# Performance work log

Hardware: AMD Instinct MI355X
Metric: run time of the kernel (lower is better)

## Reference

```python
import jax, jax.numpy as jnp
import numpy as np

N_HEADS = 16
D_MODEL = 512
HEAD_DIM = D_MODEL // N_HEADS
SCALE = 1.0 / (HEAD_DIM ** 0.5)
R = 4  # LSREF radius -> window = step = 2*r = 8


def _layernorm(x, g, b, eps=1e-5):
    m = x.mean(axis=-1, keepdims=True)
    v = x.var(axis=-1, keepdims=True)
    return (x - m) / jnp.sqrt(v + eps) * g + b


def _mha(q_in, k_in, v_in, wq, bq, wk, bk, wv, bv, wo, bo):
    # Informer FullAttention(mask_flag=False), AttentionLayer(mix=False), eval mode (no dropout)
    B, L, _ = q_in.shape
    S = k_in.shape[1]
    q = (q_in @ wq.T + bq).reshape(B, L, N_HEADS, HEAD_DIM)
    k = (k_in @ wk.T + bk).reshape(B, S, N_HEADS, HEAD_DIM)
    v = (v_in @ wv.T + bv).reshape(B, S, N_HEADS, HEAD_DIM)
    scores = jnp.einsum('blhe,bshe->bhls', q, k) * SCALE
    A = jax.nn.softmax(scores, axis=-1)
    out = jnp.einsum('bhls,bshd->blhd', A, v).reshape(B, L, D_MODEL)
    return out @ wo.T + bo


def setup_inputs() -> dict:
    key = jax.random.key(0)
    ks = jax.random.split(key, 32)
    B, L, C, GL, DFF = 4, 1024, 512, 4096, 2048

    def w(k, shape, s=0.02):
        return (jax.random.normal(k, shape, jnp.float32) * s).astype(jnp.float32)

    inp = {
        'x': jax.random.normal(ks[0], (B, L, C), jnp.float32),
        'global_feat': jax.random.normal(ks[1], (B, C, GL), jnp.float32),
        'conv_w': w(ks[2], (C, C)), 'conv_b': jnp.zeros((C,), jnp.float32),
        'sa_wq': w(ks[3], (C, C)), 'sa_bq': jnp.zeros((C,), jnp.float32),
        'sa_wk': w(ks[4], (C, C)), 'sa_bk': jnp.zeros((C,), jnp.float32),
        'sa_wv': w(ks[5], (C, C)), 'sa_bv': jnp.zeros((C,), jnp.float32),
        'sa_wo': w(ks[6], (C, C)), 'sa_bo': jnp.zeros((C,), jnp.float32),
        'ca_wq': w(ks[7], (C, C)), 'ca_bq': jnp.zeros((C,), jnp.float32),
        'ca_wk': w(ks[8], (C, C)), 'ca_bk': jnp.zeros((C,), jnp.float32),
        'ca_wv': w(ks[9], (C, C)), 'ca_bv': jnp.zeros((C,), jnp.float32),
        'ca_wo': w(ks[10], (C, C)), 'ca_bo': jnp.zeros((C,), jnp.float32),
        'ffn_w1': w(ks[11], (DFF, C)), 'ffn_b1': jnp.zeros((DFF,), jnp.float32),
        'ffn_w2': w(ks[12], (C, DFF)), 'ffn_b2': jnp.zeros((C,), jnp.float32),
        'n1_g': jnp.ones((C,), jnp.float32), 'n1_b': jnp.zeros((C,), jnp.float32),
        'n2_g': jnp.ones((C,), jnp.float32), 'n2_b': jnp.zeros((C,), jnp.float32),
        'n3_g': jnp.ones((C,), jnp.float32), 'n3_b': jnp.zeros((C,), jnp.float32),
    }
    return inp


def reference(x, global_feat, conv_w, conv_b,
              sa_wq, sa_bq, sa_wk, sa_bk, sa_wv, sa_bv, sa_wo, sa_bo,
              ca_wq, ca_bq, ca_wk, ca_bk, ca_wv, ca_bv, ca_wo, ca_bo,
              ffn_w1, ffn_b1, ffn_w2, ffn_b2,
              n1_g, n1_b, n2_g, n2_b, n3_g, n3_b):
    # --- sliding_window_gaussian: non-overlapping windows (step == window == 2r) ---
    B, C, GL = global_feat.shape
    win_sz = 2 * R
    nw = (GL - win_sz) // win_sz + 1
    win = global_feat[:, :, :nw * win_sz].reshape(B, C, nw, win_sz)
    # torch.norm over a keepdim=1 axis is just |max - min|
    res = jnp.abs(win.max(axis=-1) - win.min(axis=-1)) + 1e-6  # [B, C, nw]
    # conv1d kernel size 1 == channelwise linear, then relu
    res = jax.nn.relu(jnp.einsum('oc,bcn->bon', conv_w, res) + conv_b[None, :, None])
    cross = res  # [B, 512, nw=512] consumed as [B, S, d_model]

    # --- CrossPyramidFusion: one Informer-style layer (self-attn, cross-attn, conv FFN) ---
    h = x + _mha(x, x, x, sa_wq, sa_bq, sa_wk, sa_bk, sa_wv, sa_bv, sa_wo, sa_bo)
    h = _layernorm(h, n1_g, n1_b)
    h = h + _mha(h, cross, cross, ca_wq, ca_bq, ca_wk, ca_bk, ca_wv, ca_bv, ca_wo, ca_bo)
    h = _layernorm(h, n2_g, n2_b)
    y = jax.nn.gelu(h @ ffn_w1.T + ffn_b1, approximate=False)
    y = y @ ffn_w2.T + ffn_b2
    out = _layernorm(h + y, n3_g, n3_b)
    return out.transpose(0, 2, 1)  # [B, 512, L]
```

## Files before the change

### kernel.cpp

```cpp
#include <hip/hip_runtime.h>
#include <hip/hip_bf16.h>
#include <math.h>

#define SCALE_Q 0.25504522f

typedef unsigned short u16;
typedef unsigned int u32;
typedef __attribute__((ext_vector_type(8))) short bshort8;
typedef __attribute__((ext_vector_type(4))) short sshort4;
typedef __attribute__((ext_vector_type(4))) float f32x4;
typedef __attribute__((ext_vector_type(4))) u32 u32x4;

__device__ inline u16 f2b(float f) {
    union { float f; uint32_t u; } c;
    c.f = f;
    uint32_t u = c.u;
    return (u16)((u + 0x7fffu + ((u >> 16) & 1u)) >> 16);
}

__device__ __forceinline__ float b2f(u16 b) {
    union { u32 u; float f; } c;
    c.u = (u32)b << 16;
    return c.f;
}

__device__ __forceinline__ u32 cvtpk(float a, float b) {
    u32 r;
    asm("v_cvt_pk_bf16_f32 %0, %1, %2" : "=v"(r) : "v"(a), "v"(b));
    return r;
}

__device__ __forceinline__ float exp2c(float s) {
    float c = fminf(s, 100.f);
    float r;
    asm("v_exp_f32 %0, %1" : "=v"(r) : "v"(c));
    return r;
}

__device__ inline void gload_lds16(const void* g, void* lds) {
    __builtin_amdgcn_global_load_lds(
        (const __attribute__((address_space(1))) void*)g,
        (__attribute__((address_space(3))) void*)lds, 16, 0, 0);
}

struct WSrc { const float* p[12]; };
__global__ __launch_bounds__(256) void prep_kernel(WSrc s, u16* __restrict__ dst,
                                                   const float* __restrict__ G,
                                                   u16* __restrict__ Rt) {
    int bid = blockIdx.x;
    if (bid < 256) {
        __shared__ u16 T[64][72];
        int b = bid >> 6, c0 = ((bid >> 3) & 7) << 6, n0 = (bid & 7) << 6;
        int t = threadIdx.x;
        int n = t & 63, cq = t >> 6;
        const float* Gb = G + (long)b * 512 * 4096;
        #pragma unroll
        for (int i = 0; i < 16; i++) {
            int c = i * 4 + cq;
            const float4* p = (const float4*)(Gb + (long)(c0 + c) * 4096 + (n0 + n) * 8);
            float4 a = p[0], bb = p[1];
            float mx = fmaxf(fmaxf(fmaxf(a.x, a.y), fmaxf(a.z, a.w)),
                             fmaxf(fmaxf(bb.x, bb.y), fmaxf(bb.z, bb.w)));
            float mn = fminf(fminf(fminf(a.x, a.y), fminf(a.z, a.w)),
                             fminf(fminf(bb.x, bb.y), fminf(bb.z, bb.w)));
            T[n][c] = f2b(fabsf(mx - mn) + 1e-6f);
        }
        __syncthreads();
        int nr = t >> 2, ck = (t & 3) << 4;
        u16* o = Rt + ((long)(b * 512 + n0 + nr) << 9) + c0 + ck;
        *(bshort8*)o = *(const bshort8*)&T[nr][ck];
        *(bshort8*)(o + 8) = *(const bshort8*)&T[nr][ck + 8];
    } else {
        long e = ((long)(bid - 256) * 256 + threadIdx.x) * 4;
        if (e >= 6553600) return;
        int w; long base;
        if (e < 2359296)      { w = (int)(e >> 18); base = (long)w << 18; }
        else if (e < 3407872) { w = 9;  base = 2359296; }
        else if (e < 4456448) { w = 10; base = 3407872; }
        else                  { w = 11; base = 4456448; }
        float4 v = *(const float4*)(s.p[w] + (e - base));
        dst[e + 0] = f2b(v.x); dst[e + 1] = f2b(v.y);
        dst[e + 2] = f2b(v.z); dst[e + 3] = f2b(v.w);
    }
}

struct GArg {
    const u16* A; const u16* Bt;
    const float* bias; const u16* Rres;
    void* Cout;
    int N, K;
    long sA, sB, sC;
    u16* D1; u16* D2;
    const float* bias1; const float* bias2;
    int gx, gy;
};

template <int BIASMODE, int ACT, bool RESID, int OUTMODE>
__device__ __forceinline__ void gemm_epilogue_elem(
    float v, int row, int col, int N, long zoff,
    const float* bias, const u16* Rres, void* Cout,
    u16* D1, u16* D2, const float* bias1, const float* bias2) {
    if (OUTMODE == 3) {
        int grp = col >> 9, c = col & 511;
        float bb = (grp == 0) ? bias[c] : (grp == 1) ? bias1[c] : bias2[c];
        float vv = v + bb;
        if (grp == 0)
            ((u16*)Cout)[(long)row * 512 + c] = f2b(vv * SCALE_Q);
        else if (grp == 1)
            D1[(long)row * 512 + c] = f2b(vv);
        else
            D2[((long)((row >> 10) * 512 + c) << 10) + (row & 1023)] = f2b(vv);
    } else if (OUTMODE == 4) {
        int grp = col >> 9, c = col & 511;
        float vv = v + ((grp == 0) ? bias[c] : bias1[c]);
        if (grp == 0)
            ((u16*)Cout)[(long)row * 512 + c] = f2b(vv);
        else
            D2[((long)((row >> 9) * 512 + c) << 9) + (row & 511)] = f2b(vv);
    } else {
        if (BIASMODE == 1) v += bias[col];
        if (BIASMODE == 2) v += bias[row];
        if (ACT == 1) v = fmaxf(v, 0.f);
        if (ACT == 2) v = 0.5f * v * (1.f + erff(v * 0.70710678118654752f));
        if (ACT == 3) v *= SCALE_Q;
        if (RESID) v += b2f(Rres[(long)row * N + col]);
        long off = zoff + (long)row * N + col;
        if (OUTMODE == 1) ((u16*)Cout)[off] = f2b(v);
        else              ((float*)Cout)[off] = v;
    }
}

template <int BIASMODE, int ACT, bool RESID, int OUTMODE>
__device__ __forceinline__ void bgemm64_body(
    u16* AsB, u16* BsB, const GArg& ga, int bx, int by, int bz) {
    const u16* A  = ga.A + (long)bz * ga.sA;
    const u16* Bt = ga.Bt + (long)bz * ga.sB;
    int K = ga.K, N = ga.N;
    int tid = threadIdx.x;
    int lane = tid & 63, wv = tid >> 6;
    int wr = wv >> 1, wc = wv & 1;
    int m0 = bx * 64, n0 = by * 64;
    f32x4 acc[2][2] = {};
    int srow = lane >> 3;
    int selem = ((lane & 7) ^ srow) << 3;

    auto STAGE = [&](int buf, int k0) {
        #pragma unroll
        for (int i = 0; i < 2; i++) {
            int roff = i * 32 + wv * 8;
            gload_lds16(A + (long)(m0 + roff + srow) * K + k0 + selem,
                        (char*)(AsB + buf * 4096) + roff * 128);
            gload_lds16(Bt + (long)(n0 + roff + srow) * K + k0 + selem,
                        (char*)(BsB + buf * 4096) + roff * 128);
        }
    };

    int NT = K >> 6;
    STAGE(0, 0);
    int cur = 0;
    for (int kt = 0; kt < NT; ++kt) {
        if (kt + 1 < NT) {
            STAGE(cur ^ 1, (kt + 1) << 6);
            asm volatile("s_waitcnt vmcnt(4)\ns_barrier" ::: "memory");
        } else {
            asm volatile("s_waitcnt vmcnt(0)\ns_barrier" ::: "memory");
        }
        const char* Asc = (const char*)(AsB + cur * 4096);
        const char* Bsc = (const char*)(BsB + cur * 4096);
        #pragma unroll
        for (int ks = 0; ks < 2; ks++) {
            bshort8 af[2], bf[2];
            int kbo = ks * 64 + ((lane >> 4) << 4);
            #pragma unroll
            for (int f = 0; f < 2; f++) {
                int arow = wr * 32 + f * 16 + (lane & 15);
                af[f] = *(const bshort8*)(Asc + arow * 128 + (kbo ^ ((arow & 7) << 4)));
                int brow = wc * 32 + f * 16 + (lane & 15);
                bf[f] = *(const bshort8*)(Bsc + brow * 128 + (kbo ^ ((brow & 7) << 4)));
            }
            #pragma unroll
            for (int fi = 0; fi < 2; fi++)
                #pragma unroll
                for (int fj = 0; fj < 2; fj++)
                    acc[fi][fj] = __builtin_amdgcn_mfma_f32_16x16x32_bf16(
                        af[fi], bf[fj], acc[fi][fj], 0, 0, 0);
        }
        asm volatile("s_barrier" ::: "memory");
        cur ^= 1;
    }
    long zoff = (long)bz * ga.sC;
    #pragma unroll
    for (int fi = 0; fi < 2; fi++)
        #pragma unroll
        for (int fj = 0; fj < 2; fj++)
            #pragma unroll
            for (int r = 0; r < 4; r++) {
                int row = m0 + wr * 32 + fi * 16 + ((lane >> 4) << 2) + r;
                int col = n0 + wc * 32 + fj * 16 + (lane & 15);
                gemm_epilogue_elem<BIASMODE, ACT, RESID, OUTMODE>(
                    acc[fi][fj][r], row, col, N, zoff, ga.bias, ga.Rres, ga.Cout,
                    ga.D1, ga.D2, ga.bias1, ga.bias2);
            }
}

template <int BIASMODE, int ACT, bool RESID, int OUTMODE>
__global__ __launch_bounds__(256) void bgemm64_kernel(GArg ga) {
    __shared__ u16 As[2 * 4096];
    __shared__ u16 Bs[2 * 4096];
    bgemm64_body<BIASMODE, ACT, RESID, OUTMODE>(As, Bs, ga,
        blockIdx.x, blockIdx.y, blockIdx.z);
}

template <int B0, int A0, bool R0, int O0, int B1, int A1, bool R1, int O1>
__global__ __launch_bounds__(256) void gemm_pair_kernel(GArg a, int nblk0, GArg b) {
    __shared__ u16 As[2 * 4096];
    __shared__ u16 Bs[2 * 4096];
    int bid = blockIdx.x;
    if (bid < nblk0) {
        int xy = a.gx * a.gy;
        int bz = bid / xy, r = bid - bz * xy;
        bgemm64_body<B0, A0, R0, O0>(As, Bs, a, r % a.gx, r / a.gx, bz);
    } else {
        int bid2 = bid - nblk0;
        int xy = b.gx * b.gy;
        int bz = bid2 / xy, r = bid2 - bz * xy;
        bgemm64_body<B1, A1, R1, O1>(As, Bs, b, r % b.gx, r / b.gx, bz);
    }
}

__global__ __launch_bounds__(512) void attn_mfma_kernel(
    const u16* __restrict__ Q, const u16* __restrict__ K,
    const u16* __restrict__ Vt, u16* __restrict__ O, int L, int S) {
    __shared__ __align__(16) u16 Ks[3][2048];
    __shared__ __align__(16) u16 Vs[3][2048];
    int bh = blockIdx.x;
    int b = bh >> 4, h = bh & 15;
    int tid = threadIdx.x;
    int lane = tid & 63, wv = tid >> 6;
    int q0 = blockIdx.y * 128 + wv * 16;
    int qr = lane & 15, g = lane >> 4, g8 = g * 8;
    int kperm = 8 * (qr >> 2) + (qr & 3);
    int nt = S >> 6;

    const u16* Kb = K + (long)b * S * 512 + h * 32;
    const u16* Vb = Vt + ((long)b * 512 + h * 32) * S;
    bshort8 qf = *(const bshort8*)(Q + ((long)(b * L + q0 + qr)) * 512 + h * 32 + g8);

    const u16* src;
    long step;
    char* d0;
    if (wv < 4) {
        int rk = wv * 16 + (lane >> 2);
        int f = ((rk >> 3) & 3) ^ ((rk >> 1) & 3);
        int sc = (lane & 3) ^ f;
        src = Kb + (long)rk * 512 + sc * 8;
        step = (long)64 * 512;
        d0 = (char*)Ks[0] + wv * 1024;
    } else {
        int rv = (wv - 4) * 8 + (lane >> 3);
        int sc = (lane & 7) ^ (lane >> 3);
        src = Vb + (long)rv * S + sc * 8;
        step = 64;
        d0 = (char*)Vs[0] + (wv - 4) * 1024;
    }

    f32x4 acc0 = {}, acc1 = {}, acc2 = {};
    const bshort8 onesf = { (short)0x3F80, (short)0x3F80, (short)0x3F80, (short)0x3F80,
                            (short)0x3F80, (short)0x3F80, (short)0x3F80, (short)0x3F80 };
    int f0 = (qr >> 2) ^ ((qr >> 1) & 1);
    int f1 = f0 ^ 2;

    gload_lds16(src, d0);
    gload_lds16(src + step, d0 + 4096);
    int cur = 0;
    for (int t = 0; t < nt; ++t) {
        if (t + 2 < nt) {
            int nb = cur + 2; if (nb >= 3) nb -= 3;
            gload_lds16(src + (long)(t + 2) * step, d0 + nb * 4096);
            asm volatile("s_waitcnt vmcnt(2)\ns_barrier" ::: "memory");
        } else if (t + 1 < nt) {
            asm volatile("s_waitcnt vmcnt(1)\ns_barrier" ::: "memory");
        } else {
            asm volatile("s_waitcnt vmcnt(0)\ns_barrier" ::: "memory");
        }
        const char* Kt = (const char*)Ks[0] + cur * 4096;
        const char* Vl = (const char*)Vs[0] + cur * 4096;
        bshort8 a0 = *(const bshort8*)(Kt + kperm * 64 + ((g ^ f0) << 4));
        bshort8 a1 = *(const bshort8*)(Kt + (kperm + 4) * 64 + ((g ^ f1) << 4));
        bshort8 a2 = *(const bshort8*)(Kt + (kperm + 32) * 64 + ((g ^ f0) << 4));
        bshort8 a3 = *(const bshort8*)(Kt + (kperm + 36) * 64 + ((g ^ f1) << 4));
        bshort8 v00 = *(const bshort8*)(Vl + qr * 128 + ((g ^ (qr & 7)) << 4));
        bshort8 v01 = *(const bshort8*)(Vl + qr * 128 + (((g + 4) ^ (qr & 7)) << 4));
        bshort8 v10 = *(const bshort8*)(Vl + (16 + qr) * 128 + ((g ^ (qr & 7)) << 4));
        bshort8 v11 = *(const bshort8*)(Vl + (16 + qr) * 128 + (((g + 4) ^ (qr & 7)) << 4));
        f32x4 zz = {0.f, 0.f, 0.f, 0.f};
        f32x4 st0 = __builtin_amdgcn_mfma_f32_16x16x32_bf16(a0, qf, zz, 0, 0, 0);
        f32x4 st1 = __builtin_amdgcn_mfma_f32_16x16x32_bf16(a1, qf, zz, 0, 0, 0);
        f32x4 st2 = __builtin_amdgcn_mfma_f32_16x16x32_bf16(a2, qf, zz, 0, 0, 0);
        f32x4 st3 = __builtin_amdgcn_mfma_f32_16x16x32_bf16(a3, qf, zz, 0, 0, 0);
        float p0[4], p1[4], p2[4], p3[4];
        #pragma unroll
        for (int r = 0; r < 4; r++) {
            p0[r] = exp2c(st0[r]);
            p1[r] = exp2c(st1[r]);
            p2[r] = exp2c(st2[r]);
            p3[r] = exp2c(st3[r]);
        }
        u32x4 P0 = { cvtpk(p0[0], p0[1]), cvtpk(p0[2], p0[3]),
                     cvtpk(p1[0], p1[1]), cvtpk(p1[2], p1[3]) };
        u32x4 P1 = { cvtpk(p2[0], p2[1]), cvtpk(p2[2], p2[3]),
                     cvtpk(p3[0], p3[1]), cvtpk(p3[2], p3[3]) };
        bshort8 pf0 = *(bshort8*)&P0;
        bshort8 pf1 = *(bshort8*)&P1;
        acc0 = __builtin_amdgcn_mfma_f32_16x16x32_bf16(v00, pf0, acc0, 0, 0, 0);
        acc0 = __builtin_amdgcn_mfma_f32_16x16x32_bf16(v01, pf1, acc0, 0, 0, 0);
        acc1 = __builtin_amdgcn_mfma_f32_16x16x32_bf16(v10, pf0, acc1, 0, 0, 0);
        acc1 = __builtin_amdgcn_mfma_f32_16x16x32_bf16(v11, pf1, acc1, 0, 0, 0);
        acc2 = __builtin_amdgcn_mfma_f32_16x16x32_bf16(onesf, pf0, acc2, 0, 0, 0);
        acc2 = __builtin_amdgcn_mfma_f32_16x16x32_bf16(onesf, pf1, acc2, 0, 0, 0);
        asm volatile("s_barrier" ::: "memory");
        cur = (cur == 2) ? 0 : cur + 1;
    }

    float inv = 1.f / acc2[0];
    u16* op = O + ((long)(b * L + q0 + qr)) * 512 + h * 32 + g * 4;
    sshort4 o0, o1;
    #pragma unroll
    for (int r = 0; r < 4; r++) {
        o0[r] = (short)f2b(acc0[r] * inv);
        o1[r] = (short)f2b(acc1[r] * inv);
    }
    *(sshort4*)op = o0;
    *(sshort4*)(op + 16) = o1;
}

__global__ __launch_bounds__(256) void ln_kernel(const u16* __restrict__ X,
                                                 const float* __restrict__ g,
                                                 const float* __restrict__ bt,
                                                 u16* __restrict__ Yb) {
    int row = blockIdx.x;
    int t = threadIdx.x;
    u32 pack = ((const u32*)(X + (long)row * 512))[t];
    float x0 = b2f((u16)(pack & 0xffff));
    float x1 = b2f((u16)(pack >> 16));
    float s = x0 + x1, ss = x0 * x0 + x1 * x1;
    #pragma unroll
    for (int off = 32; off > 0; off >>= 1) {
        s += __shfl_down(s, off);
        ss += __shfl_down(ss, off);
    }
    __shared__ float sred[4], ssred[4];
    int wid = t >> 6;
    if ((t & 63) == 0) { sred[wid] = s; ssred[wid] = ss; }
    __syncthreads();
    float ts = sred[0] + sred[1] + sred[2] + sred[3];
    float tss = ssred[0] + ssred[1] + ssred[2] + ssred[3];
    float mean = ts * (1.f / 512.f);
    float var = tss * (1.f / 512.f) - mean * mean;
    float rstd = rsqrtf(var + 1e-5f);
    float y0 = (x0 - mean) * rstd * g[2 * t] + bt[2 * t];
    float y1 = (x1 - mean) * rstd * g[2 * t + 1] + bt[2 * t + 1];
    ((u32*)(Yb + (long)row * 512))[t] = cvtpk(y0, y1);
}

__global__ __launch_bounds__(256) void ln_stats_kernel(const u16* __restrict__ X,
                                                       float2* __restrict__ stats) {
    int row = blockIdx.x * 4 + (threadIdx.x >> 6);
    int lane = threadIdx.x & 63;
    bshort8 v = *(const bshort8*)(X + (long)row * 512 + lane * 8);
    float s = 0.f, ss = 0.f;
    #pragma unroll
    for (int i = 0; i < 8; i++) {
        float f = b2f((u16)v[i]);
        s += f;
        ss += f * f;
    }
    #pragma unroll
    for (int off = 32; off > 0; off >>= 1) {
        s += __shfl_down(s, off);
        ss += __shfl_down(ss, off);
    }
    if (lane == 0) {
        float mean = s * (1.f / 512.f);
        float var = ss * (1.f / 512.f) - mean * mean;
        stats[row] = make_float2(mean, rsqrtf(var + 1e-5f));
    }
}

__global__ __launch_bounds__(256) void ln_trans_kernel(
    const u16* __restrict__ X, const float2* __restrict__ stats,
    const float* __restrict__ g, const float* __restrict__ bt,
    float* __restrict__ Y) {
    __shared__ u16 T[64][66];
    int b = blockIdx.z, l0 = blockIdx.x * 64, c0 = blockIdx.y * 64;
    int t = threadIdx.x;
    int col = t & 63, rq = t >> 6;
    #pragma unroll
    for (int i = 0; i < 16; i++) {
        int row = i * 4 + rq;
        T[row][col] = X[((long)(b * 1024 + l0 + row)) * 512 + c0 + col];
    }
    __syncthreads();
    float2 mr = stats[b * 1024 + l0 + col];
    #pragma unroll
    for (int i = 0; i < 16; i++) {
        int c = i * 4 + rq;
        float val = (b2f(T[col][c]) - mr.x) * mr.y * g[c0 + c] + bt[c0 + c];
        Y[((long)(b * 512 + c0 + c)) * 1024 + l0 + col] = val;
    }
}

extern "C" void kernel_launch(void* const* d_in, const int* in_sizes, int n_in,
                              void* d_out, int out_size, void* d_ws, size_t ws_size,
                              hipStream_t stream) {
    const float* x      = (const float*)d_in[0];
    const float* gfeat  = (const float*)d_in[1];
    const float* conv_w = (const float*)d_in[2];
    const float* conv_b = (const float*)d_in[3];
    const float* sa_wq = (const float*)d_in[4];
    const float* sa_bq = (const float*)d_in[5];
    const float* sa_bk = (const float*)d_in[7];
    const float* sa_bv = (const float*)d_in[9];
    const float* sa_bo = (const float*)d_in[11];
    const float* ca_bq = (const float*)d_in[13];
    const float* ca_bk = (const float*)d_in[15];
    const float* ca_bv = (const float*)d_in[17];
    const float* ca_bo = (const float*)d_in[19];
    const float* ffn_b1 = (const float*)d_in[21];
    const float* ffn_b2 = (const float*)d_in[23];
    const float* n1_g = (const float*)d_in[24];
    const float* n1_b = (const float*)d_in[25];
    const float* n2_g = (const float*)d_in[26];
    const float* n2_b = (const float*)d_in[27];
    const float* n3_g = (const float*)d_in[28];
    const float* n3_b = (const float*)d_in[29];
    (void)ws_size; (void)n_in; (void)in_sizes; (void)out_size;

    const long M_ = 1048576;
    float* W0 = (float*)d_ws;
    u16* hb    = (u16*)W0;
    u16* U = (u16*)(W0 + 4 * M_);
    u16* qb     = U;
    u16* kb     = U + 2 * M_;
    u16* vtb    = U + 4 * M_;
    u16* k2b    = U + 6 * M_;
    u16* v2tb   = U + 7 * M_;
    u16* attb   = U + 8 * M_;
    u16* hnb    = U + 10 * M_;
    u16* midb   = U + 12 * M_;
    u16* wsb    = U + 20 * M_;
    u16* res_tb = U + 27 * M_;
    u16* crossb = U + 28 * M_;

    float2* ln3_stats = (float2*)res_tb;

    const u16* conv_wb = wsb;
    const u16* sa_wqb = wsb + 262144;
    const u16* sa_wob = wsb + 1048576;
    const u16* ca_wqb = wsb + 1310720;
    const u16* ca_wkb = wsb + 1572864;
    const u16* ca_wob = wsb + 2097152;
    const u16* ffn1b = wsb + 2359296, *ffn2b = wsb + 3407872;
    const u16* xb = wsb + 4456448;

    WSrc ws;
    ws.p[0] = conv_w; ws.p[1] = sa_wq; ws.p[2] = (const float*)d_in[6];
    ws.p[3] = (const float*)d_in[8]; ws.p[4] = (const float*)d_in[10];
    ws.p[5] = (const float*)d_in[12]; ws.p[6] = (const float*)d_in[14];
    ws.p[7] = (const float*)d_in[16]; ws.p[8] = (const float*)d_in[18];
    ws.p[9] = (const float*)d_in[20]; ws.p[10] = (const float*)d_in[22];
    ws.p[11] = x;
    prep_kernel<<<6656, 256, 0, stream>>>(ws, wsb, gfeat, res_tb);

    GArg convA = { conv_wb, res_tb, conv_b, nullptr, crossb, 512, 512,
                   0, 262144, 262144, nullptr, nullptr, nullptr, nullptr, 8, 8 };
    GArg qkvA  = { xb, sa_wqb, sa_bq, nullptr, qb, 1536, 512,
                   0, 0, 0, kb, vtb, sa_bk, sa_bv, 64, 24 };
    gemm_pair_kernel<2, 1, false, 1, 1, 0, false, 3><<<1792, 256, 0, stream>>>(
        convA, 256, qkvA);

    attn_mfma_kernel<<<dim3(64, 8), 512, 0, stream>>>(qb, kb, vtb, attb, 1024, 1024);

    GArg op1 = { attb, sa_wob, sa_bo, xb, hb, 512, 512,
                 0, 0, 0, nullptr, nullptr, nullptr, nullptr, 64, 8 };
    bgemm64_kernel<1, 0, true, 1><<<dim3(64, 8), 256, 0, stream>>>(op1);

    ln_kernel<<<4096, 256, 0, stream>>>(hb, n1_g, n1_b, hnb);

    GArg qA  = { hnb, ca_wqb, ca_bq, nullptr, qb, 512, 512,
                 0, 0, 0, nullptr, nullptr, nullptr, nullptr, 64, 8 };
    GArg kvA = { crossb, ca_wkb, ca_bk, nullptr, k2b, 1024, 512,
                 0, 0, 0, nullptr, v2tb, ca_bv, nullptr, 32, 16 };
    gemm_pair_kernel<1, 3, false, 1, 1, 0, false, 4><<<1024, 256, 0, stream>>>(
        qA, 512, kvA);

    attn_mfma_kernel<<<dim3(64, 8), 512, 0, stream>>>(qb, k2b, v2tb, attb, 1024, 512);

    GArg op2 = { attb, ca_wob, ca_bo, hnb, hb, 512, 512,
                 0, 0, 0, nullptr, nullptr, nullptr, nullptr, 64, 8 };
    bgemm64_kernel<1, 0, true, 1><<<dim3(64, 8), 256, 0, stream>>>(op2);

    ln_kernel<<<4096, 256, 0, stream>>>(hb, n2_g, n2_b, hnb);

    GArg f1 = { hnb, ffn1b, ffn_b1, nullptr, midb, 2048, 512,
                0, 0, 0, nullptr, nullptr, nullptr, nullptr, 64, 32 };
    bgemm64_kernel<1, 2, false, 1><<<dim3(64, 32), 256, 0, stream>>>(f1);

    GArg f2 = { midb, ffn2b, ffn_b2, hnb, hb, 512, 2048,
                0, 0, 0, nullptr, nullptr, nullptr, nullptr, 64, 8 };
    bgemm64_kernel<1, 0, true, 1><<<dim3(64, 8), 256, 0, stream>>>(f2);

    ln_stats_kernel<<<1024, 256, 0, stream>>>(hb, ln3_stats);
    ln_trans_kernel<<<dim3(16, 8, 4), 256, 0, stream>>>(
        hb, ln3_stats, n3_g, n3_b, (float*)d_out);
}
```

Before: 159.4 us.

## Overlap weight conversion with GEMMs and cross K/V GEMM with self-attention

The weight fp32-to-bf16 conversion is split. Only the weights the first GEMM pair needs (conv, sa_wq, and the x/ffn range) are converted in the prep kernel. The remaining weights are converted by extra blocks appended to the conv+QKV GEMM launch. The cross-attention K/V projection moves into the self-attention launch as extra blocks, where 4 of the 8 waves run the GEMM and the other waves idle on matching barriers. This cuts serialization and tail gaps between launches, but adds heterogeneous blocks, larger shared memory in the attention kernel, and half-idle GEMM blocks.

```diff
diff --git a/kernel.cpp b/kernel.cpp
--- a/kernel.cpp
+++ b/kernel.cpp
@@ -44,9 +44,20 @@
 }
 
 struct WSrc { const float* p[12]; };
-__global__ __launch_bounds__(256) void prep_kernel(WSrc s, u16* __restrict__ dst,
-                                                   const float* __restrict__ G,
-                                                   u16* __restrict__ Rt) {
+__device__ __forceinline__ void conv4(const WSrc& s, u16* __restrict__ dst, long e) {
+    int w; long base;
+    if (e < 2359296)      { w = (int)(e >> 18); base = (long)w << 18; }
+    else if (e < 3407872) { w = 9;  base = 2359296; }
+    else if (e < 4456448) { w = 10; base = 3407872; }
+    else                  { w = 11; base = 4456448; }
+    float4 v = *(const float4*)(s.p[w] + (e - base));
+    dst[e + 0] = f2b(v.x); dst[e + 1] = f2b(v.y);
+    dst[e + 2] = f2b(v.z); dst[e + 3] = f2b(v.w);
+}
+
+__global__ __launch_bounds__(256) void prep1_kernel(WSrc s, u16* __restrict__ dst,
+                                                    const float* __restrict__ G,
+                                                    u16* __restrict__ Rt) {
     int bid = blockIdx.x;
     if (bid < 256) {
         __shared__ u16 T[64][72];
@@ -71,16 +82,10 @@
         *(bshort8*)o = *(const bshort8*)&T[nr][ck];
         *(bshort8*)(o + 8) = *(const bshort8*)&T[nr][ck + 8];
     } else {
-        long e = ((long)(bid - 256) * 256 + threadIdx.x) * 4;
-        if (e >= 6553600) return;
-        int w; long base;
-        if (e < 2359296)      { w = (int)(e >> 18); base = (long)w << 18; }
-        else if (e < 3407872) { w = 9;  base = 2359296; }
-        else if (e < 4456448) { w = 10; base = 3407872; }
-        else                  { w = 11; base = 4456448; }
-        float4 v = *(const float4*)(s.p[w] + (e - base));
-        dst[e + 0] = f2b(v.x); dst[e + 1] = f2b(v.y);
-        dst[e + 2] = f2b(v.z); dst[e + 3] = f2b(v.w);
+        int i = bid - 256;
+        long e = (i < 1024) ? (long)i * 1024 + threadIdx.x * 4
+                            : 4456448 + (long)(i - 1024) * 1024 + threadIdx.x * 4;
+        conv4(s, dst, e);
     }
 }
 
@@ -212,7 +217,8 @@
 }
 
 template <int B0, int A0, bool R0, int O0, int B1, int A1, bool R1, int O1>
-__global__ __launch_bounds__(256) void gemm_pair_kernel(GArg a, int nblk0, GArg b) {
+__global__ __launch_bounds__(256) void pair_conv_kernel(
+    GArg a, int nblk0, GArg b, int nblk1, WSrc s, u16* __restrict__ dst) {
     __shared__ u16 As[2 * 4096];
     __shared__ u16 Bs[2 * 4096];
     int bid = blockIdx.x;
@@ -220,24 +226,26 @@
         int xy = a.gx * a.gy;
         int bz = bid / xy, r = bid - bz * xy;
         bgemm64_body<B0, A0, R0, O0>(As, Bs, a, r % a.gx, r / a.gx, bz);
-    } else {
+    } else if (bid < nblk1) {
         int bid2 = bid - nblk0;
         int xy = b.gx * b.gy;
         int bz = bid2 / xy, r = bid2 - bz * xy;
         bgemm64_body<B1, A1, R1, O1>(As, Bs, b, r % b.gx, r / b.gx, bz);
-    }
-}
-
-__global__ __launch_bounds__(512) void attn_mfma_kernel(
+    } else {
+        long e = 1048576 + (long)(bid - nblk1) * 1024 + threadIdx.x * 4;
+        conv4(s, dst, e);
+    }
+}
+
+__device__ __forceinline__ void attn_body(
+    u16* KsB, u16* VsB,
     const u16* __restrict__ Q, const u16* __restrict__ K,
-    const u16* __restrict__ Vt, u16* __restrict__ O, int L, int S) {
-    __shared__ __align__(16) u16 Ks[3][2048];
-    __shared__ __align__(16) u16 Vs[3][2048];
-    int bh = blockIdx.x;
+    const u16* __restrict__ Vt, u16* __restrict__ O, int L, int S,
+    int bh, int qy) {
     int b = bh >> 4, h = bh & 15;
     int tid = threadIdx.x;
     int lane = tid & 63, wv = tid >> 6;
-    int q0 = blockIdx.y * 128 + wv * 16;
+    int q0 = qy * 128 + wv * 16;
     int qr = lane & 15, g = lane >> 4, g8 = g * 8;
     int kperm = 8 * (qr >> 2) + (qr & 3);
     int nt = S >> 6;
@@ -255,13 +263,13 @@
         int sc = (lane & 3) ^ f;
         src = Kb + (long)rk * 512 + sc * 8;
         step = (long)64 * 512;
-        d0 = (char*)Ks[0] + wv * 1024;
+        d0 = (char*)KsB + wv * 1024;
     } else {
         int rv = (wv - 4) * 8 + (lane >> 3);
         int sc = (lane & 7) ^ (lane >> 3);
         src = Vb + (long)rv * S + sc * 8;
         step = 64;
-        d0 = (char*)Vs[0] + (wv - 4) * 1024;
+        d0 = (char*)VsB + (wv - 4) * 1024;
     }
 
     f32x4 acc0 = {}, acc1 = {}, acc2 = {};
@@ -283,8 +291,8 @@
         } else {
             asm volatile("s_waitcnt vmcnt(0)\ns_barrier" ::: "memory");
         }
-        const char* Kt = (const char*)Ks[0] + cur * 4096;
-        const char* Vl = (const char*)Vs[0] + cur * 4096;
+        const char* Kt = (const char*)KsB + cur * 4096;
+        const char* Vl = (const char*)VsB + cur * 4096;
         bshort8 a0 = *(const bshort8*)(Kt + kperm * 64 + ((g ^ f0) << 4));
         bshort8 a1 = *(const bshort8*)(Kt + (kperm + 4) * 64 + ((g ^ f1) << 4));
         bshort8 a2 = *(const bshort8*)(Kt + (kperm + 32) * 64 + ((g ^ f0) << 4));
@@ -332,6 +340,38 @@
     }
     *(sshort4*)op = o0;
     *(sshort4*)(op + 16) = o1;
+}
+
+__global__ __launch_bounds__(512) void attn_mfma_kernel(
+    const u16* __restrict__ Q, const u16* __restrict__ K,
+    const u16* __restrict__ Vt, u16* __restrict__ O, int L, int S) {
+    __shared__ __align__(16) u16 SH[12288];
+    attn_body(SH, SH + 6144, Q, K, Vt, O, L, S, blockIdx.x, blockIdx.y);
+}
+
+template <int B1, int A1, bool R1, int O1>
+__global__ __launch_bounds__(512) void attn_gemm_kernel(
+    const u16* __restrict__ Q, const u16* __restrict__ K,
+    const u16* __restrict__ Vt, u16* __restrict__ O, int L, int S,
+    int nAttn, GArg g) {
+    __shared__ __align__(16) u16 SH[16384];
+    int bid = blockIdx.x;
+    if (bid < nAttn) {
+        attn_body(SH, SH + 6144, Q, K, Vt, O, L, S, bid & 63, bid >> 6);
+    } else {
+        int bid2 = bid - nAttn;
+        if ((threadIdx.x >> 6) < 4) {
+            int xy = g.gx * g.gy;
+            int bz = bid2 / xy, r = bid2 - bz * xy;
+            bgemm64_body<B1, A1, R1, O1>(SH, SH + 8192, g, r % g.gx, r / g.gx, bz);
+        } else {
+            int NT = g.K >> 6;
+            for (int kt = 0; kt < NT; ++kt) {
+                __builtin_amdgcn_s_barrier();
+                __builtin_amdgcn_s_barrier();
+            }
+        }
+    }
 }
 
 __global__ __launch_bounds__(256) void ln_kernel(const u16* __restrict__ X,
@@ -470,16 +510,20 @@
     ws.p[7] = (const float*)d_in[16]; ws.p[8] = (const float*)d_in[18];
     ws.p[9] = (const float*)d_in[20]; ws.p[10] = (const float*)d_in[22];
     ws.p[11] = x;
-    prep_kernel<<<6656, 256, 0, stream>>>(ws, wsb, gfeat, res_tb);
+
+    prep1_kernel<<<3328, 256, 0, stream>>>(ws, wsb, gfeat, res_tb);
 
     GArg convA = { conv_wb, res_tb, conv_b, nullptr, crossb, 512, 512,
                    0, 262144, 262144, nullptr, nullptr, nullptr, nullptr, 8, 8 };
     GArg qkvA  = { xb, sa_wqb, sa_bq, nullptr, qb, 1536, 512,
                    0, 0, 0, kb, vtb, sa_bk, sa_bv, 64, 24 };
-    gemm_pair_kernel<2, 1, false, 1, 1, 0, false, 3><<<1792, 256, 0, stream>>>(
-        convA, 256, qkvA);
-
-    attn_mfma_kernel<<<dim3(64, 8), 512, 0, stream>>>(qb, kb, vtb, attb, 1024, 1024);
+    pair_conv_kernel<2, 1, false, 1, 1, 0, false, 3><<<5120, 256, 0, stream>>>(
+        convA, 256, qkvA, 1792, ws, wsb);
+
+    GArg kvA = { crossb, ca_wkb, ca_bk, nullptr, k2b, 1024, 512,
+                 0, 0, 0, nullptr, v2tb, ca_bv, nullptr, 32, 16 };
+    attn_gemm_kernel<1, 0, false, 4><<<1024, 512, 0, stream>>>(
+        qb, kb, vtb, attb, 1024, 1024, 512, kvA);
 
     GArg op1 = { attb, sa_wob, sa_bo, xb, hb, 512, 512,
                  0, 0, 0, nullptr, nullptr, nullptr, nullptr, 64, 8 };
@@ -489,10 +533,7 @@
 
     GArg qA  = { hnb, ca_wqb, ca_bq, nullptr, qb, 512, 512,
                  0, 0, 0, nullptr, nullptr, nullptr, nullptr, 64, 8 };
-    GArg kvA = { crossb, ca_wkb, ca_bk, nullptr, k2b, 1024, 512,
-                 0, 0, 0, nullptr, v2tb, ca_bv, nullptr, 32, 16 };
-    gemm_pair_kernel<1, 3, false, 1, 1, 0, false, 4><<<1024, 256, 0, stream>>>(
-        qA, 512, kvA);
+    bgemm64_kernel<1, 3, false, 1><<<dim3(64, 8), 256, 0, stream>>>(qA);
 
     attn_mfma_kernel<<<dim3(64, 8), 512, 0, stream>>>(qb, k2b, v2tb, attb, 1024, 512);
 
```

Measured after the change: 159.5 us. About the same (+0.0%).
